# Optimization experiments

Hardware: AMD Instinct MI355X
Metric: run time of the kernel (lower is better)

Reference implementation:

```python
import jax, jax.numpy as jnp
import numpy as np

N = 20000      # nodes
E = 320000     # edges (before self loops)
IN = 128       # in_channels
HID = 64       # hid_channels
H = 4          # in_head
OUT = 16       # out_channels (classes)
SLOPE = 0.2    # GATv2 leaky_relu negative_slope default


def setup_inputs() -> dict:
    key = jax.random.key(0)
    ks = jax.random.split(key, 40)
    d = {}
    d["x"] = jax.random.normal(ks[0], (N, IN), jnp.float32)
    src = jax.random.randint(ks[1], (E,), 0, N)
    dst = jax.random.randint(ks[2], (E,), 0, N)
    d["edge_index"] = jnp.stack([src, dst]).astype(jnp.int32)
    # (in_ch, out_ch_per_head, heads) for the 4 GATv2Conv layers
    dims = [(IN, HID, H), (H * HID, HID, H), (H * HID, HID, H), (H * HID, OUT, 1)]
    ki = 3
    for li, (ic, oc, h) in enumerate(dims, 1):
        sc = 1.0 / np.sqrt(ic)
        d[f"w{li}l"] = jax.random.normal(ks[ki], (h * oc, ic), jnp.float32) * sc; ki += 1
        d[f"b{li}l"] = jnp.zeros((h * oc,), jnp.float32)
        d[f"w{li}r"] = jax.random.normal(ks[ki], (h * oc, ic), jnp.float32) * sc; ki += 1
        d[f"b{li}r"] = jnp.zeros((h * oc,), jnp.float32)
        d[f"a{li}"] = jax.random.normal(ks[ki], (h, oc), jnp.float32) * (1.0 / np.sqrt(oc)); ki += 1
        # output bias: [h*oc] if concat else [oc]; layer 4 is concat=False
        d[f"bo{li}"] = jnp.zeros((h * oc if li < 4 else oc,), jnp.float32)
    return d


def gatv2_layer(x, src, dst, wl, bl, wr, br, att, bias, heads, oc, concat):
    n = x.shape[0]
    xl = (x @ wl.T + bl).reshape(n, heads, oc)   # source transform
    xr = (x @ wr.T + br).reshape(n, heads, oc)   # target transform
    # per-edge GATv2 attention logit: a^T LeakyReLU(x_l[src] + x_r[dst])
    e = jax.nn.leaky_relu(xl[src] + xr[dst], SLOPE)          # [E,H,C]
    logits = jnp.einsum('ehc,hc->eh', e, att)                # [E,H]
    # segment softmax over incoming edges of each dst node
    m = jax.ops.segment_max(logits, dst, num_segments=n)     # [N,H]
    ex = jnp.exp(logits - m[dst])
    den = jax.ops.segment_sum(ex, dst, num_segments=n)
    alpha = ex / den[dst]                                    # [E,H]
    out = jax.ops.segment_sum(alpha[..., None] * xl[src], dst, num_segments=n)  # [N,H,C]
    out = out.reshape(n, heads * oc) if concat else out.mean(axis=1)
    return out + bias


def reference(x, edge_index,
              w1l, b1l, w1r, b1r, a1, bo1,
              w2l, b2l, w2r, b2r, a2, bo2,
              w3l, b3l, w3r, b3r, a3, bo3,
              w4l, b4l, w4r, b4r, a4, bo4):
    n = x.shape[0]
    loop = jnp.arange(n, dtype=edge_index.dtype)
    src = jnp.concatenate([edge_index[0], loop])  # PyG GATv2Conv adds self loops
    dst = jnp.concatenate([edge_index[1], loop])
    h = gatv2_layer(x, src, dst, w1l, b1l, w1r, b1r, a1, bo1, H, HID, True)
    h = jax.nn.relu(h)
    h = gatv2_layer(h, src, dst, w2l, b2l, w2r, b2r, a2, bo2, H, HID, True)
    h = jax.nn.relu(h)
    h = gatv2_layer(h, src, dst, w3l, b3l, w3r, b3r, a3, bo3, H, HID, True)
    h = jax.nn.relu(h)
    h = gatv2_layer(h, src, dst, w4l, b4l, w4r, b4r, a4, bo4, 1, OUT, False)
    return h
```

## Files before the change

kernel.cpp:

```cpp
#include <hip/hip_runtime.h>
#include <hip/hip_bf16.h>
#include <math.h>

#define NNODES 20000
#define NEDGES 320000
#define ETOT   (NEDGES + NNODES)
#define SLOPE  0.2f
#define MAXDEG 96

typedef __attribute__((ext_vector_type(8))) short bf16x8;
typedef __attribute__((ext_vector_type(4))) float f32x4;

__device__ inline unsigned short bfbits(float f) {
    __hip_bfloat16 h = __float2bfloat16(f);
    unsigned short u;
    __builtin_memcpy(&u, &h, 2);
    return u;
}
__device__ inline float bf2f(unsigned short u) {
    __hip_bfloat16 h;
    __builtin_memcpy(&h, &u, 2);
    return __bfloat162float(h);
}

__device__ inline void gload_lds16(const unsigned short* g, unsigned short* s) {
    __builtin_amdgcn_global_load_lds(
        (const __attribute__((address_space(1))) unsigned int*)g,
        (__attribute__((address_space(3))) unsigned int*)s, 16, 0, 0);
}

__global__ void slab_fill(const int* __restrict__ ei, int* __restrict__ fill,
                          int* __restrict__ slab) {
    int idx = blockIdx.x * blockDim.x + threadIdx.x;
    if (idx >= ETOT) return;
    int src, dst;
    if (idx < NEDGES) { src = ei[idx]; dst = ei[NEDGES + idx]; }
    else              { src = idx - NEDGES; dst = src; }
    int pos = atomicAdd(&fill[dst], 1);
    if (pos < MAXDEG) slab[dst * MAXDEG + pos] = src;
}

__global__ void convert_x(const float* __restrict__ x, unsigned short* __restrict__ Ap) {
    int idx = blockIdx.x * 256 + threadIdx.x;
    if (idx >= NNODES * 128) return;
    int m = idx >> 7, k = idx & 127;
    float f = x[idx];
    unsigned short hi = bfbits(f);
    unsigned short lo = bfbits(f - bf2f(hi));
    unsigned short* row = Ap + (size_t)m * 384;
    row[k] = hi; row[128 + k] = lo; row[256 + k] = hi;
}

__global__ void convert_w(const float* __restrict__ w0, const float* __restrict__ w1,
                          unsigned short* __restrict__ Wp, int K, int n0, int ntot) {
    int idx = blockIdx.x * 256 + threadIdx.x;
    if (idx >= ntot * K) return;
    int n = idx / K, k = idx - n * K;
    float f = (n < n0) ? w0[n * K + k] : w1[(n - n0) * K + k];
    unsigned short hi = bfbits(f);
    unsigned short lo = bfbits(f - bf2f(hi));
    unsigned short* row = Wp + (size_t)n * 3 * K;
    row[k] = hi; row[K + k] = hi; row[2 * K + k] = lo;
}

template <int NOUT>
__global__ __launch_bounds__(256) void gemm_mfma(
    const unsigned short* __restrict__ Ap, int KP,
    const unsigned short* __restrict__ Wp,
    const float* __restrict__ bias0, const float* __restrict__ bias1,
    float* __restrict__ O0, float* __restrict__ O1)
{
    __shared__ unsigned short Alds[8 * 512];
    __shared__ unsigned short Wlds[8 * 512];

    int m0, nblk;
    if constexpr (NOUT == 512) {
        const int bid = blockIdx.x;
        const int xcd = bid & 7;
        const int k   = bid >> 3;
        nblk = k & 3;
        const int g = (k >> 2) * 8 + xcd;
        if (g >= (NNODES + 127) / 128) return;
        m0 = g * 128;
    } else {
        nblk = 0;
        m0 = blockIdx.x * 128;
    }
    const int n0 = nblk * 128;

    const int tid = threadIdx.x;
    const int l   = tid & 63;
    const int wid = tid >> 6;
    const int wr  = wid >> 1;
    const int wc  = wid & 1;

    const int srow = l & 15;
    const int skb  = l >> 4;

    int arow0 = m0 + wid * 16 + srow;
    int arow1 = arow0 + 64;
    arow0 = min(arow0, NNODES - 1);
    arow1 = min(arow1, NNODES - 1);
    const unsigned short* ag0 = Ap + (size_t)arow0 * KP + skb * 8;
    const unsigned short* ag1 = Ap + (size_t)arow1 * KP + skb * 8;
    int nrow0 = min(n0 + wid * 16 + srow, NOUT - 1);
    int nrow1 = min(n0 + wid * 16 + srow + 64, NOUT - 1);
    const unsigned short* wg0 = Wp + (size_t)nrow0 * KP + skb * 8;
    const unsigned short* wg1 = Wp + (size_t)nrow1 * KP + skb * 8;

    unsigned short* al0 = &Alds[(0 * 4 + wid) * 512];
    unsigned short* al1 = &Alds[(1 * 4 + wid) * 512];
    unsigned short* wl0 = &Wlds[(0 * 4 + wid) * 512];
    unsigned short* wl1 = &Wlds[(1 * 4 + wid) * 512];

    const unsigned short* ard = &Alds[(wr * 4) * 512 + l * 8];
    const unsigned short* wrd = &Wlds[(wc * 4) * 512 + l * 8];

    f32x4 acc[4][4];
    #pragma unroll
    for (int i = 0; i < 4; i++)
        #pragma unroll
        for (int j = 0; j < 4; j++)
            acc[i][j] = (f32x4){0.f, 0.f, 0.f, 0.f};

    for (int k0 = 0; k0 < KP; k0 += 32) {
        gload_lds16(ag0 + k0, al0);
        gload_lds16(ag1 + k0, al1);
        gload_lds16(wg0 + k0, wl0);
        gload_lds16(wg1 + k0, wl1);
        __syncthreads();

        bf16x8 a0 = *(const bf16x8*)(ard + 0 * 512);
        bf16x8 a1 = *(const bf16x8*)(ard + 1 * 512);
        bf16x8 a2 = *(const bf16x8*)(ard + 2 * 512);
        bf16x8 a3 = *(const bf16x8*)(ard + 3 * 512);
        bf16x8 b0 = *(const bf16x8*)(wrd + 0 * 512);
        bf16x8 b1 = *(const bf16x8*)(wrd + 1 * 512);
        bf16x8 b2 = *(const bf16x8*)(wrd + 2 * 512);
        bf16x8 b3 = *(const bf16x8*)(wrd + 3 * 512);

        acc[0][0] = __builtin_amdgcn_mfma_f32_16x16x32_bf16(a0, b0, acc[0][0], 0, 0, 0);
        acc[0][1] = __builtin_amdgcn_mfma_f32_16x16x32_bf16(a0, b1, acc[0][1], 0, 0, 0);
        acc[0][2] = __builtin_amdgcn_mfma_f32_16x16x32_bf16(a0, b2, acc[0][2], 0, 0, 0);
        acc[0][3] = __builtin_amdgcn_mfma_f32_16x16x32_bf16(a0, b3, acc[0][3], 0, 0, 0);
        acc[1][0] = __builtin_amdgcn_mfma_f32_16x16x32_bf16(a1, b0, acc[1][0], 0, 0, 0);
        acc[1][1] = __builtin_amdgcn_mfma_f32_16x16x32_bf16(a1, b1, acc[1][1], 0, 0, 0);
        acc[1][2] = __builtin_amdgcn_mfma_f32_16x16x32_bf16(a1, b2, acc[1][2], 0, 0, 0);
        acc[1][3] = __builtin_amdgcn_mfma_f32_16x16x32_bf16(a1, b3, acc[1][3], 0, 0, 0);
        acc[2][0] = __builtin_amdgcn_mfma_f32_16x16x32_bf16(a2, b0, acc[2][0], 0, 0, 0);
        acc[2][1] = __builtin_amdgcn_mfma_f32_16x16x32_bf16(a2, b1, acc[2][1], 0, 0, 0);
        acc[2][2] = __builtin_amdgcn_mfma_f32_16x16x32_bf16(a2, b2, acc[2][2], 0, 0, 0);
        acc[2][3] = __builtin_amdgcn_mfma_f32_16x16x32_bf16(a2, b3, acc[2][3], 0, 0, 0);
        acc[3][0] = __builtin_amdgcn_mfma_f32_16x16x32_bf16(a3, b0, acc[3][0], 0, 0, 0);
        acc[3][1] = __builtin_amdgcn_mfma_f32_16x16x32_bf16(a3, b1, acc[3][1], 0, 0, 0);
        acc[3][2] = __builtin_amdgcn_mfma_f32_16x16x32_bf16(a3, b2, acc[3][2], 0, 0, 0);
        acc[3][3] = __builtin_amdgcn_mfma_f32_16x16x32_bf16(a3, b3, acc[3][3], 0, 0, 0);

        __syncthreads();
    }

    if constexpr (NOUT == 512) {
        const bool  left = (nblk < 2);
        float*       O   = left ? O0 : O1;
        const float* bs  = left ? bias0 : bias1;
        const int   cb   = (nblk & 1) * 128;
        #pragma unroll
        for (int mi = 0; mi < 4; mi++) {
            int r0 = m0 + wr * 64 + mi * 16 + (l >> 4) * 4;
            #pragma unroll
            for (int ni = 0; ni < 4; ni++) {
                int c = cb + wc * 64 + ni * 16 + (l & 15);
                float bv = bs[c];
                #pragma unroll
                for (int r = 0; r < 4; r++) {
                    int m = r0 + r;
                    if (m < NNODES) O[(size_t)m * 256 + c] = acc[mi][ni][r] + bv;
                }
            }
        }
    } else {
        #pragma unroll
        for (int mi = 0; mi < 4; mi++) {
            int r0 = m0 + wr * 64 + mi * 16 + (l >> 4) * 4;
            #pragma unroll
            for (int ni = 0; ni < 4; ni++) {
                int c = wc * 64 + ni * 16 + (l & 15);
                if (c >= 32) continue;
                float bv = (c < 16) ? bias0[c] : bias1[c - 16];
                #pragma unroll
                for (int r = 0; r < 4; r++) {
                    int m = r0 + r;
                    if (m < NNODES) O0[(size_t)m * 32 + c] = acc[mi][ni][r] + bv;
                }
            }
        }
    }
}

__device__ inline float edge_score(float4 v, float4 xrv, float4 attv) {
    float tx = v.x + xrv.x; tx = (tx > 0.f) ? tx : SLOPE * tx;
    float ty = v.y + xrv.y; ty = (ty > 0.f) ? ty : SLOPE * ty;
    float tz = v.z + xrv.z; tz = (tz > 0.f) ? tz : SLOPE * tz;
    float tw = v.w + xrv.w; tw = (tw > 0.f) ? tw : SLOPE * tw;
    float s = attv.x * tx + attv.y * ty + attv.z * tz + attv.w * tw;
    s += __shfl_xor(s, 1, 64);
    s += __shfl_xor(s, 2, 64);
    s += __shfl_xor(s, 4, 64);
    s += __shfl_xor(s, 8, 64);
    return s;
}

__device__ inline void sm_update(float s, float4 v, float& m, float& den, float4& acc) {
    float d = s - m;
    bool  r = d > 8.f;
    float e = __expf(r ? -d : d);
    float sc = r ? e : 1.f;
    float pw = r ? 1.f : e;
    m = r ? s : m;
    den = den * sc + pw;
    acc.x = acc.x * sc + pw * v.x;
    acc.y = acc.y * sc + pw * v.y;
    acc.z = acc.z * sc + pw * v.z;
    acc.w = acc.w * sc + pw * v.w;
}

__device__ inline void sm_merge(float& m0, float& den0, float4& acc0,
                                float m1, float den1, float4 acc1) {
    float nm = fmaxf(m0, m1);
    float sa = __expf(m0 - nm);
    float sb = __expf(m1 - nm);
    den0 = den0 * sa + den1 * sb;
    acc0.x = acc0.x * sa + acc1.x * sb;
    acc0.y = acc0.y * sa + acc1.y * sb;
    acc0.z = acc0.z * sa + acc1.z * sb;
    acc0.w = acc0.w * sa + acc1.w * sb;
    m0 = nm;
}

__global__ __launch_bounds__(64) void gat_attn_node(
    const float* __restrict__ xl, const float* __restrict__ xr,
    const float* __restrict__ att, const float* __restrict__ bo,
    const int* __restrict__ fill, const int* __restrict__ slab,
    unsigned short* __restrict__ outp)
{
    const int lane = threadIdx.x;
    const int node = blockIdx.x;

    const unsigned laneoff = (unsigned)lane << 4;
    const char*    xlb     = (const char*)xl;

    const float4 attv = *(const float4*)&att[lane * 4];
    const float4 xrv  = *(const float4*)((const char*)xr + ((unsigned)node << 10) + laneoff);
    const float4 bov  = *(const float4*)&bo[lane * 4];

    const int  deg = min(fill[node], MAXDEG);
    const int* sl  = slab + node * MAXDEG;

    float  m0 = -1e30f, m1 = -1e30f, m2 = -1e30f, m3 = -1e30f;
    float  d0 = 0.f, d1 = 0.f, d2 = 0.f, d3 = 0.f;
    float4 a0 = make_float4(0.f, 0.f, 0.f, 0.f);
    float4 a1 = a0, a2 = a0, a3 = a0;

    int p = 0;
    for (; p + 4 <= deg; p += 4) {
        int4 s4 = *(const int4*)&sl[p];
        float4 v0 = *(const float4*)(xlb + (((unsigned)s4.x << 10) + laneoff));
        float4 v1 = *(const float4*)(xlb + (((unsigned)s4.y << 10) + laneoff));
        float4 v2 = *(const float4*)(xlb + (((unsigned)s4.z << 10) + laneoff));
        float4 v3 = *(const float4*)(xlb + (((unsigned)s4.w << 10) + laneoff));
        float sc0 = edge_score(v0, xrv, attv);
        float sc1 = edge_score(v1, xrv, attv);
        float sc2 = edge_score(v2, xrv, attv);
        float sc3 = edge_score(v3, xrv, attv);
        sm_update(sc0, v0, m0, d0, a0);
        sm_update(sc1, v1, m1, d1, a1);
        sm_update(sc2, v2, m2, d2, a2);
        sm_update(sc3, v3, m3, d3, a3);
    }
    for (; p < deg; ++p) {
        int src = sl[p];
        float4 v = *(const float4*)(xlb + (((unsigned)src << 10) + laneoff));
        float s = edge_score(v, xrv, attv);
        sm_update(s, v, m0, d0, a0);
    }

    sm_merge(m0, d0, a0, m1, d1, a1);
    sm_merge(m2, d2, a2, m3, d3, a3);
    sm_merge(m0, d0, a0, m2, d2, a2);

    float4 o;
    o.x = fmaxf(a0.x / d0 + bov.x, 0.f);
    o.y = fmaxf(a0.y / d0 + bov.y, 0.f);
    o.z = fmaxf(a0.z / d0 + bov.z, 0.f);
    o.w = fmaxf(a0.w / d0 + bov.w, 0.f);

    unsigned short* row = outp + (size_t)node * 768 + lane * 4;
    ushort4 hv, lv;
    hv.x = bfbits(o.x); hv.y = bfbits(o.y); hv.z = bfbits(o.z); hv.w = bfbits(o.w);
    lv.x = bfbits(o.x - bf2f(hv.x));
    lv.y = bfbits(o.y - bf2f(hv.y));
    lv.z = bfbits(o.z - bf2f(hv.z));
    lv.w = bfbits(o.w - bf2f(hv.w));
    *(ushort4*)(row)       = hv;
    *(ushort4*)(row + 256) = lv;
    *(ushort4*)(row + 512) = hv;
}

__global__ __launch_bounds__(64) void gat_attn_final(
    const float* __restrict__ O32,
    const float* __restrict__ att, const float* __restrict__ bo,
    const int* __restrict__ fill, const int* __restrict__ slab,
    float* __restrict__ out)
{
    const int lane = threadIdx.x;
    const int sub  = lane >> 4;
    const int c    = lane & 15;

    const int node = blockIdx.x * 4 + sub;
    if (node >= NNODES) return;

    const unsigned coff = (unsigned)c << 2;
    const char*    ob   = (const char*)O32;

    const float attc = att[c];
    const float xrc  = *(const float*)(ob + (((unsigned)node << 7) + 64 + coff));

    const int  deg = min(fill[node], MAXDEG);
    const int* sl  = slab + node * MAXDEG;

    float m0 = -1e30f, m1 = -1e30f, d0 = 0.f, d1 = 0.f, a0 = 0.f, a1 = 0.f;

    int p = 0;
    for (; p + 2 <= deg; p += 2) {
        int srcA = sl[p];
        int srcB = sl[p + 1];
        float vA = *(const float*)(ob + (((unsigned)srcA << 7) + coff));
        float vB = *(const float*)(ob + (((unsigned)srcB << 7) + coff));
        float tA = vA + xrc; tA = (tA > 0.f) ? tA : SLOPE * tA;
        float tB = vB + xrc; tB = (tB > 0.f) ? tB : SLOPE * tB;
        float sA = attc * tA;
        float sB = attc * tB;
        sA += __shfl_xor(sA, 1, 64);  sB += __shfl_xor(sB, 1, 64);
        sA += __shfl_xor(sA, 2, 64);  sB += __shfl_xor(sB, 2, 64);
        sA += __shfl_xor(sA, 4, 64);  sB += __shfl_xor(sB, 4, 64);
        sA += __shfl_xor(sA, 8, 64);  sB += __shfl_xor(sB, 8, 64);
        {
            float dd = sA - m0; bool r = dd > 8.f;
            float e = __expf(r ? -dd : dd);
            float sc = r ? e : 1.f, pw = r ? 1.f : e;
            m0 = r ? sA : m0;
            d0 = d0 * sc + pw;
            a0 = a0 * sc + pw * vA;
        }
        {
            float dd = sB - m1; bool r = dd > 8.f;
            float e = __expf(r ? -dd : dd);
            float sc = r ? e : 1.f, pw = r ? 1.f : e;
            m1 = r ? sB : m1;
            d1 = d1 * sc + pw;
            a1 = a1 * sc + pw * vB;
        }
    }
    if (p < deg) {
        int src = sl[p];
        float v = *(const float*)(ob + (((unsigned)src << 7) + coff));
        float t = v + xrc; t = (t > 0.f) ? t : SLOPE * t;
        float s = attc * t;
        s += __shfl_xor(s, 1, 64);
        s += __shfl_xor(s, 2, 64);
        s += __shfl_xor(s, 4, 64);
        s += __shfl_xor(s, 8, 64);
        float dd = s - m0; bool r = dd > 8.f;
        float e = __expf(r ? -dd : dd);
        float sc = r ? e : 1.f, pw = r ? 1.f : e;
        m0 = r ? s : m0;
        d0 = d0 * sc + pw;
        a0 = a0 * sc + pw * v;
    }

    float nm = fmaxf(m0, m1);
    float sa = __expf(m0 - nm);
    float sb = __expf(m1 - nm);
    float den = d0 * sa + d1 * sb;
    out[(size_t)node * 16 + c] = (a0 * sa + a1 * sb) / den + bo[c];
}

extern "C" void kernel_launch(void* const* d_in, const int* in_sizes, int n_in,
                              void* d_out, int out_size, void* d_ws, size_t ws_size,
                              hipStream_t stream)
{
    const float* x   = (const float*)d_in[0];
    const int*   ei  = (const int*)d_in[1];
    const float* w1l = (const float*)d_in[2];  const float* b1l = (const float*)d_in[3];
    const float* w1r = (const float*)d_in[4];  const float* b1r = (const float*)d_in[5];
    const float* a1  = (const float*)d_in[6];  const float* bo1 = (const float*)d_in[7];
    const float* w2l = (const float*)d_in[8];  const float* b2l = (const float*)d_in[9];
    const float* w2r = (const float*)d_in[10]; const float* b2r = (const float*)d_in[11];
    const float* a2  = (const float*)d_in[12]; const float* bo2 = (const float*)d_in[13];
    const float* w3l = (const float*)d_in[14]; const float* b3l = (const float*)d_in[15];
    const float* w3r = (const float*)d_in[16]; const float* b3r = (const float*)d_in[17];
    const float* a3  = (const float*)d_in[18]; const float* bo3 = (const float*)d_in[19];
    const float* w4l = (const float*)d_in[20]; const float* b4l = (const float*)d_in[21];
    const float* w4r = (const float*)d_in[22]; const float* b4r = (const float*)d_in[23];
    const float* a4  = (const float*)d_in[24]; const float* bo4 = (const float*)d_in[25];

    char* ws = (char*)d_ws;
    auto carve = [&](size_t bytes) {
        void* p = ws;
        ws += (bytes + 255) & ~(size_t)255;
        return p;
    };
    unsigned short* Ap = (unsigned short*)carve((size_t)NNODES * 768 * sizeof(unsigned short));
    float* xl = (float*)carve((size_t)NNODES * 256 * sizeof(float));
    float* xr = (float*)carve((size_t)NNODES * 256 * sizeof(float));
    float* O32 = xl;
    unsigned short* Wp1 = (unsigned short*)carve((size_t)512 * 384 * sizeof(unsigned short));
    unsigned short* Wp2 = (unsigned short*)carve((size_t)512 * 768 * sizeof(unsigned short));
    unsigned short* Wp3 = (unsigned short*)carve((size_t)512 * 768 * sizeof(unsigned short));
    unsigned short* Wp4 = (unsigned short*)carve((size_t)32 * 768 * sizeof(unsigned short));
    int* fill = (int*)carve((size_t)NNODES * sizeof(int));
    int* slab = (int*)carve((size_t)NNODES * MAXDEG * sizeof(int));

    const int eblocks = (ETOT + 255) / 256;

    convert_x<<<(NNODES * 128 + 255) / 256, 256, 0, stream>>>(x, Ap);
    convert_w<<<(512 * 128 + 255) / 256, 256, 0, stream>>>(w1l, w1r, Wp1, 128, 256, 512);
    convert_w<<<(512 * 256 + 255) / 256, 256, 0, stream>>>(w2l, w2r, Wp2, 256, 256, 512);
    convert_w<<<(512 * 256 + 255) / 256, 256, 0, stream>>>(w3l, w3r, Wp3, 256, 256, 512);
    convert_w<<<(32 * 256 + 255) / 256, 256, 0, stream>>>(w4l, w4r, Wp4, 256, 16, 32);

    hipMemsetAsync(fill, 0, (size_t)NNODES * sizeof(int), stream);
    slab_fill<<<eblocks, 256, 0, stream>>>(ei, fill, slab);

    const int g512 = 640;

    gemm_mfma<512><<<g512, 256, 0, stream>>>(Ap, 384, Wp1, b1l, b1r, xl, xr);
    gat_attn_node<<<NNODES, 64, 0, stream>>>(xl, xr, a1, bo1, fill, slab, Ap);

    gemm_mfma<512><<<g512, 256, 0, stream>>>(Ap, 768, Wp2, b2l, b2r, xl, xr);
    gat_attn_node<<<NNODES, 64, 0, stream>>>(xl, xr, a2, bo2, fill, slab, Ap);

    gemm_mfma<512><<<g512, 256, 0, stream>>>(Ap, 768, Wp3, b3l, b3r, xl, xr);
    gat_attn_node<<<NNODES, 64, 0, stream>>>(xl, xr, a3, bo3, fill, slab, Ap);

    gemm_mfma<32><<<(NNODES + 127) / 128, 256, 0, stream>>>(Ap, 768, Wp4, b4l, b4r, O32, O32);
    gat_attn_final<<<(NNODES + 3) / 4, 64, 0, stream>>>(O32, a4, bo4, fill, slab, (float*)d_out);
}
```

Baseline: 336.6 us.

## Software-pipeline edge gathers, add fast-path softmax, pack two nodes per block

The attention kernel now issues the gathers for the next batch of four neighbours before computing on the current batch, overlapping load latency with math. A wave-uniform fast path skips the rescale logic when no running max needs updating. LeakyReLU becomes a fmax. Both attention kernels pack two wavefronts per 128-thread block to cut block count. The prefetch raises register pressure, and the extra branch adds a wave vote on every batch.

```diff
diff --git a/kernel.cpp b/kernel.cpp
--- a/kernel.cpp
+++ b/kernel.cpp
@@ -198,10 +198,10 @@
 }
 
 __device__ inline float edge_score(float4 v, float4 xrv, float4 attv) {
-    float tx = v.x + xrv.x; tx = (tx > 0.f) ? tx : SLOPE * tx;
-    float ty = v.y + xrv.y; ty = (ty > 0.f) ? ty : SLOPE * ty;
-    float tz = v.z + xrv.z; tz = (tz > 0.f) ? tz : SLOPE * tz;
-    float tw = v.w + xrv.w; tw = (tw > 0.f) ? tw : SLOPE * tw;
+    float tx = v.x + xrv.x; tx = fmaxf(tx, SLOPE * tx);
+    float ty = v.y + xrv.y; ty = fmaxf(ty, SLOPE * ty);
+    float tz = v.z + xrv.z; tz = fmaxf(tz, SLOPE * tz);
+    float tw = v.w + xrv.w; tw = fmaxf(tw, SLOPE * tw);
     float s = attv.x * tx + attv.y * ty + attv.z * tz + attv.w * tw;
     s += __shfl_xor(s, 1, 64);
     s += __shfl_xor(s, 2, 64);
@@ -237,14 +237,15 @@
     m0 = nm;
 }
 
-__global__ __launch_bounds__(64) void gat_attn_node(
+__global__ __launch_bounds__(128) void gat_attn_node(
     const float* __restrict__ xl, const float* __restrict__ xr,
     const float* __restrict__ att, const float* __restrict__ bo,
     const int* __restrict__ fill, const int* __restrict__ slab,
     unsigned short* __restrict__ outp)
 {
-    const int lane = threadIdx.x;
-    const int node = blockIdx.x;
+    const int lane = threadIdx.x & 63;
+    const int node = blockIdx.x * 2 + (threadIdx.x >> 6);
+    if (node >= NNODES) return;
 
     const unsigned laneoff = (unsigned)lane << 4;
     const char*    xlb     = (const char*)xl;
@@ -261,25 +262,54 @@
     float4 a0 = make_float4(0.f, 0.f, 0.f, 0.f);
     float4 a1 = a0, a2 = a0, a3 = a0;
 
+    auto gather = [&](int src) -> float4 {
+        return *(const float4*)(xlb + (((unsigned)src << 10) + laneoff));
+    };
+
+    auto batch = [&](float4 v0, float4 v1, float4 v2, float4 v3) {
+        float s0 = edge_score(v0, xrv, attv);
+        float s1 = edge_score(v1, xrv, attv);
+        float s2 = edge_score(v2, xrv, attv);
+        float s3 = edge_score(v3, xrv, attv);
+        bool need = (s0 - m0 > 8.f) | (s1 - m1 > 8.f) | (s2 - m2 > 8.f) | (s3 - m3 > 8.f);
+        if (!__any(need)) {
+            float p0 = __expf(s0 - m0);
+            float p1 = __expf(s1 - m1);
+            float p2 = __expf(s2 - m2);
+            float p3 = __expf(s3 - m3);
+            d0 += p0; d1 += p1; d2 += p2; d3 += p3;
+            a0.x += p0 * v0.x; a0.y += p0 * v0.y; a0.z += p0 * v0.z; a0.w += p0 * v0.w;
+            a1.x += p1 * v1.x; a1.y += p1 * v1.y; a1.z += p1 * v1.z; a1.w += p1 * v1.w;
+            a2.x += p2 * v2.x; a2.y += p2 * v2.y; a2.z += p2 * v2.z; a2.w += p2 * v2.w;
+            a3.x += p3 * v3.x; a3.y += p3 * v3.y; a3.z += p3 * v3.z; a3.w += p3 * v3.w;
+        } else {
+            sm_update(s0, v0, m0, d0, a0);
+            sm_update(s1, v1, m1, d1, a1);
+            sm_update(s2, v2, m2, d2, a2);
+            sm_update(s3, v3, m3, d3, a3);
+        }
+    };
+
+    float4 v0, v1, v2, v3;
     int p = 0;
+    if (deg >= 4) {
+        int4 s4 = *(const int4*)sl;
+        v0 = gather(s4.x); v1 = gather(s4.y);
+        v2 = gather(s4.z); v3 = gather(s4.w);
+        p = 4;
+    }
     for (; p + 4 <= deg; p += 4) {
         int4 s4 = *(const int4*)&sl[p];
-        float4 v0 = *(const float4*)(xlb + (((unsigned)s4.x << 10) + laneoff));
-        float4 v1 = *(const float4*)(xlb + (((unsigned)s4.y << 10) + laneoff));
-        float4 v2 = *(const float4*)(xlb + (((unsigned)s4.z << 10) + laneoff));
-        float4 v3 = *(const float4*)(xlb + (((unsigned)s4.w << 10) + laneoff));
-        float sc0 = edge_score(v0, xrv, attv);
-        float sc1 = edge_score(v1, xrv, attv);
-        float sc2 = edge_score(v2, xrv, attv);
-        float sc3 = edge_score(v3, xrv, attv);
-        sm_update(sc0, v0, m0, d0, a0);
-        sm_update(sc1, v1, m1, d1, a1);
-        sm_update(sc2, v2, m2, d2, a2);
-        sm_update(sc3, v3, m3, d3, a3);
-    }
+        float4 w0 = gather(s4.x);
+        float4 w1 = gather(s4.y);
+        float4 w2 = gather(s4.z);
+        float4 w3 = gather(s4.w);
+        batch(v0, v1, v2, v3);
+        v0 = w0; v1 = w1; v2 = w2; v3 = w3;
+    }
+    if (deg >= 4) batch(v0, v1, v2, v3);
     for (; p < deg; ++p) {
-        int src = sl[p];
-        float4 v = *(const float4*)(xlb + (((unsigned)src << 10) + laneoff));
+        float4 v = gather(sl[p]);
         float s = edge_score(v, xrv, attv);
         sm_update(s, v, m0, d0, a0);
     }
@@ -306,17 +336,17 @@
     *(ushort4*)(row + 512) = hv;
 }
 
-__global__ __launch_bounds__(64) void gat_attn_final(
+__global__ __launch_bounds__(128) void gat_attn_final(
     const float* __restrict__ O32,
     const float* __restrict__ att, const float* __restrict__ bo,
     const int* __restrict__ fill, const int* __restrict__ slab,
     float* __restrict__ out)
 {
-    const int lane = threadIdx.x;
+    const int lane = threadIdx.x & 63;
     const int sub  = lane >> 4;
     const int c    = lane & 15;
 
-    const int node = blockIdx.x * 4 + sub;
+    const int node = (blockIdx.x * 2 + (threadIdx.x >> 6)) * 4 + sub;
     if (node >= NNODES) return;
 
     const unsigned coff = (unsigned)c << 2;
@@ -336,8 +366,8 @@
         int srcB = sl[p + 1];
         float vA = *(const float*)(ob + (((unsigned)srcA << 7) + coff));
         float vB = *(const float*)(ob + (((unsigned)srcB << 7) + coff));
-        float tA = vA + xrc; tA = (tA > 0.f) ? tA : SLOPE * tA;
-        float tB = vB + xrc; tB = (tB > 0.f) ? tB : SLOPE * tB;
+        float tA = vA + xrc; tA = fmaxf(tA, SLOPE * tA);
+        float tB = vB + xrc; tB = fmaxf(tB, SLOPE * tB);
         float sA = attc * tA;
         float sB = attc * tB;
         sA += __shfl_xor(sA, 1, 64);  sB += __shfl_xor(sB, 1, 64);
@@ -364,7 +394,7 @@
     if (p < deg) {
         int src = sl[p];
         float v = *(const float*)(ob + (((unsigned)src << 7) + coff));
-        float t = v + xrc; t = (t > 0.f) ? t : SLOPE * t;
+        float t = v + xrc; t = fmaxf(t, SLOPE * t);
         float s = attc * t;
         s += __shfl_xor(s, 1, 64);
         s += __shfl_xor(s, 2, 64);
@@ -433,16 +463,17 @@
     slab_fill<<<eblocks, 256, 0, stream>>>(ei, fill, slab);
 
     const int g512 = 640;
+    const int ablocks = (NNODES + 1) / 2;
 
     gemm_mfma<512><<<g512, 256, 0, stream>>>(Ap, 384, Wp1, b1l, b1r, xl, xr);
-    gat_attn_node<<<NNODES, 64, 0, stream>>>(xl, xr, a1, bo1, fill, slab, Ap);
+    gat_attn_node<<<ablocks, 128, 0, stream>>>(xl, xr, a1, bo1, fill, slab, Ap);
 
     gemm_mfma<512><<<g512, 256, 0, stream>>>(Ap, 768, Wp2, b2l, b2r, xl, xr);
-    gat_attn_node<<<NNODES, 64, 0, stream>>>(xl, xr, a2, bo2, fill, slab, Ap);
+    gat_attn_node<<<ablocks, 128, 0, stream>>>(xl, xr, a2, bo2, fill, slab, Ap);
 
     gemm_mfma<512><<<g512, 256, 0, stream>>>(Ap, 768, Wp3, b3l, b3r, xl, xr);
-    gat_attn_node<<<NNODES, 64, 0, stream>>>(xl, xr, a3, bo3, fill, slab, Ap);
+    gat_attn_node<<<ablocks, 128, 0, stream>>>(xl, xr, a3, bo3, fill, slab, Ap);
 
     gemm_mfma<32><<<(NNODES + 127) / 128, 256, 0, stream>>>(Ap, 768, Wp4, b4l, b4r, O32, O32);
-    gat_attn_final<<<(NNODES + 3) / 4, 64, 0, stream>>>(O32, a4, bo4, fill, slab, (float*)d_out);
-}
+    gat_attn_final<<<(NNODES + 7) / 8, 128, 0, stream>>>(O32, a4, bo4, fill, slab, (float*)d_out);
+}
```

Measured after the change: 336.7 us. About the same (+0.0%).
